# Optimization experiments

Hardware: AMD Instinct MI355X
Metric: run time of the kernel (lower is better)

## Reference

```python
import jax, jax.numpy as jnp
import numpy as np

B, L, D = 4, 1024, 256
N_PER, N_HYP = 48, 16  # n_oscillators=64, n_hyperbolic=16
K = N_PER + N_HYP


def _mlp(x, w1, b1, w2, b2):
    # torch nn.Linear: y = x @ W.T + b; GELU is exact (erf) by default
    h = jax.nn.gelu(x @ w1.T + b1, approximate=False)
    return h @ w2.T + b2


def setup_inputs() -> dict:
    key = jax.random.key(0)
    ks = iter(jax.random.split(key, 32))

    def lin(o, i):
        return jax.random.normal(next(ks), (o, i), jnp.float32) * 0.02

    def bias(o):
        return jnp.zeros((o,), jnp.float32)

    inp = {"x": jax.random.normal(next(ks), (B, L, D), jnp.float32)}
    # key/query periodic phase MLPs: Linear(D,D) -> GELU -> Linear(D,N_PER)
    inp.update(kp_w1=lin(D, D), kp_b1=bias(D), kp_w2=lin(N_PER, D), kp_b2=bias(N_PER))
    inp.update(qp_w1=lin(D, D), qp_b1=bias(D), qp_w2=lin(N_PER, D), qp_b2=bias(N_PER))
    # key/query hyperbolic MLPs: Linear(D,D) -> GELU -> Linear(D, 2*N_HYP)
    inp.update(kh_w1=lin(D, D), kh_b1=bias(D), kh_w2=lin(2 * N_HYP, D), kh_b2=bias(2 * N_HYP))
    inp.update(qh_w1=lin(D, D), qh_b1=bias(D), qh_w2=lin(2 * N_HYP, D), qh_b2=bias(2 * N_HYP))
    # value projection and output (LayerNorm + Linear)
    inp.update(v_w=lin(D, D), v_b=bias(D))
    inp.update(ln_g=jnp.ones((D,), jnp.float32), ln_b=jnp.zeros((D,), jnp.float32))
    inp.update(out_w=lin(D, D), out_b=bias(D))
    return inp


def reference(x, kp_w1, kp_b1, kp_w2, kp_b2, qp_w1, qp_b1, qp_w2, qp_b2,
              kh_w1, kh_b1, kh_w2, kh_b2, qh_w1, qh_b1, qh_w2, qh_b2,
              v_w, v_b, ln_g, ln_b, out_w, out_b):
    Bx, Lx, Dx = x.shape

    # periodic (flat torus) phasors: unit-magnitude
    key_p = jnp.tanh(_mlp(x, kp_w1, kp_b1, kp_w2, kp_b2)) * jnp.pi   # (B,L,N_PER)
    query_p = jnp.tanh(_mlp(x, qp_w1, qp_b1, qp_w2, qp_b2)) * jnp.pi
    key_phasor_p = jnp.exp(1j * key_p.astype(jnp.complex64))
    query_phasor_p = jnp.exp(1j * query_p.astype(jnp.complex64))

    # hyperbolic (Poincare-disk) phasors: amplitude = 1 - |z|
    key_h = jnp.tanh(_mlp(x, kh_w1, kh_b1, kh_w2, kh_b2)).reshape(Bx, Lx, N_HYP, 2) * 0.9
    query_h = jnp.tanh(_mlp(x, qh_w1, qh_b1, qh_w2, qh_b2)).reshape(Bx, Lx, N_HYP, 2) * 0.9
    key_ang = jnp.arctan2(key_h[..., 1], key_h[..., 0])
    query_ang = jnp.arctan2(query_h[..., 1], query_h[..., 0])
    key_amp = 1.0 - jnp.sqrt(jnp.sum(key_h * key_h, axis=-1))
    query_amp = 1.0 - jnp.sqrt(jnp.sum(query_h * query_h, axis=-1))
    key_phasor_h = key_amp * jnp.exp(1j * key_ang.astype(jnp.complex64))
    query_phasor_h = query_amp * jnp.exp(1j * query_ang.astype(jnp.complex64))

    key_phasor = jnp.concatenate([key_phasor_p, key_phasor_h], axis=-1)    # (B,L,K)
    query_phasor = jnp.concatenate([query_phasor_p, query_phasor_h], axis=-1)

    V = (x @ v_w.T + v_b).astype(jnp.complex64)                            # (B,L,D)

    # bind: outer product per timestep, cumsum over L (linear-attention scan)
    bound = key_phasor[..., :, None] * V[..., None, :]                     # (B,L,K,D) complex
    memory = jnp.cumsum(bound, axis=1)
    retrieved = jnp.real(jnp.sum(memory * jnp.conj(query_phasor)[..., None], axis=2))  # (B,L,D)

    positions = jnp.arange(1, Lx + 1, dtype=jnp.float32)
    norm = jnp.sqrt(positions * float(K))[None, :, None]
    r = retrieved / norm

    # to_out: LayerNorm(D) -> Linear(D,D)
    mu = jnp.mean(r, axis=-1, keepdims=True)
    var = jnp.mean(jnp.square(r - mu), axis=-1, keepdims=True)
    r_ln = (r - mu) / jnp.sqrt(var + 1e-5) * ln_g + ln_b
    return x + (r_ln @ out_w.T + out_b)
```

## Files before the change

### kernel.cpp

```cpp
#include <hip/hip_runtime.h>
#include <math.h>


#define Bn 4
#define Ln 1024
#define BLn 4096

typedef __attribute__((ext_vector_type(8))) short bf16x8;
typedef __attribute__((ext_vector_type(4))) float f32x4;

__device__ inline ushort f2bf(float f) {
  union { float f; uint u; } x; x.f = f;
  uint r = x.u + 0x7fffu + ((x.u >> 16) & 1u);
  return (ushort)(r >> 16);
}
__device__ inline uint pk2(float a, float b) {
  return (uint)f2bf(a) | ((uint)f2bf(b) << 16);
}

struct G1Prob { const float* X; const float* W; const float* bias; void* Y; int act; };
struct G1Args { G1Prob p[5]; };

__global__ __launch_bounds__(256) void gemm1(G1Args args) {
  const G1Prob p = args.p[blockIdx.z];
  __shared__ ushort As[64 * 40];
  __shared__ ushort Bs[64 * 40];
  const int tid = threadIdx.x;
  const int m0 = blockIdx.x * 64, n0 = blockIdx.y * 64;
  const int lane = tid & 63, wave = tid >> 6;
  const int wr = wave >> 1, wc = wave & 1;
  const int fr = lane & 15, quad = lane >> 4;
  f32x4 acc[2][2];
#pragma unroll
  for (int i = 0; i < 2; i++)
#pragma unroll
    for (int j = 0; j < 2; j++) acc[i][j] = (f32x4){0.f, 0.f, 0.f, 0.f};

  const int srow = tid >> 2, sch = (tid & 3) * 8;
  for (int k0 = 0; k0 < 256; k0 += 32) {
    float4 a0 = *(const float4*)(p.X + (size_t)(m0 + srow) * 256 + k0 + sch);
    float4 a1 = *(const float4*)(p.X + (size_t)(m0 + srow) * 256 + k0 + sch + 4);
    float4 b0 = *(const float4*)(p.W + (size_t)(n0 + srow) * 256 + k0 + sch);
    float4 b1 = *(const float4*)(p.W + (size_t)(n0 + srow) * 256 + k0 + sch + 4);
    uint4 pa = { pk2(a0.x, a0.y), pk2(a0.z, a0.w), pk2(a1.x, a1.y), pk2(a1.z, a1.w) };
    uint4 pb = { pk2(b0.x, b0.y), pk2(b0.z, b0.w), pk2(b1.x, b1.y), pk2(b1.z, b1.w) };
    *(uint4*)&As[srow * 40 + sch] = pa;
    *(uint4*)&Bs[srow * 40 + sch] = pb;
    __syncthreads();
    bf16x8 fa0 = *(const bf16x8*)&As[(wr * 32 + fr) * 40 + quad * 8];
    bf16x8 fa1 = *(const bf16x8*)&As[(wr * 32 + 16 + fr) * 40 + quad * 8];
    bf16x8 fb0 = *(const bf16x8*)&Bs[(wc * 32 + fr) * 40 + quad * 8];
    bf16x8 fb1 = *(const bf16x8*)&Bs[(wc * 32 + 16 + fr) * 40 + quad * 8];
    acc[0][0] = __builtin_amdgcn_mfma_f32_16x16x32_bf16(fa0, fb0, acc[0][0], 0, 0, 0);
    acc[0][1] = __builtin_amdgcn_mfma_f32_16x16x32_bf16(fa0, fb1, acc[0][1], 0, 0, 0);
    acc[1][0] = __builtin_amdgcn_mfma_f32_16x16x32_bf16(fa1, fb0, acc[1][0], 0, 0, 0);
    acc[1][1] = __builtin_amdgcn_mfma_f32_16x16x32_bf16(fa1, fb1, acc[1][1], 0, 0, 0);
    __syncthreads();
  }
#pragma unroll
  for (int i = 0; i < 2; i++)
#pragma unroll
    for (int j = 0; j < 2; j++) {
      int col = n0 + wc * 32 + j * 16 + fr;
      float bv = p.bias[col];
      if (p.act == 4) {
        int rowg0 = m0 + wr * 32 + i * 16 + quad * 4;
        ushort4 st;
        st.x = f2bf(acc[i][j][0] + bv);
        st.y = f2bf(acc[i][j][1] + bv);
        st.z = f2bf(acc[i][j][2] + bv);
        st.w = f2bf(acc[i][j][3] + bv);
        *(ushort4*)((ushort*)p.Y + (size_t)col * 4096 + rowg0) = st;
      } else {
#pragma unroll
        for (int r = 0; r < 4; r++) {
          int rowg = m0 + wr * 32 + i * 16 + quad * 4 + r;
          float o = acc[i][j][r] + bv;
          o = 0.5f * o * (1.0f + erff(o * 0.70710678118654752f));
          ((ushort*)p.Y)[(size_t)rowg * 256 + col] = f2bf(o);
        }
      }
    }
}

struct G2Prob { const ushort* X; const float* W; const float* bias; float* Y;
                int Nreal; float scale; };
struct G2Args { G2Prob p[4]; };

__global__ __launch_bounds__(256) void gemm2f(G2Args args) {
  const G2Prob p = args.p[blockIdx.z];
  __shared__ ushort As[64 * 40];
  __shared__ ushort Bs[64 * 40];
  const int tid = threadIdx.x;
  const int m0 = blockIdx.x * 64;
  const int lane = tid & 63, wave = tid >> 6;
  const int wr = wave >> 1, wc = wave & 1;
  const int fr = lane & 15, quad = lane >> 4;
  f32x4 acc[2][2];
#pragma unroll
  for (int i = 0; i < 2; i++)
#pragma unroll
    for (int j = 0; j < 2; j++) acc[i][j] = (f32x4){0.f, 0.f, 0.f, 0.f};

  const int srow = tid >> 2, sch = (tid & 3) * 8;
  for (int k0 = 0; k0 < 256; k0 += 32) {
    uint4 pa = *(const uint4*)(p.X + (size_t)(m0 + srow) * 256 + k0 + sch);
    float4 b0 = {0.f,0.f,0.f,0.f}, b1 = {0.f,0.f,0.f,0.f};
    if (srow < p.Nreal) {
      b0 = *(const float4*)(p.W + (size_t)srow * 256 + k0 + sch);
      b1 = *(const float4*)(p.W + (size_t)srow * 256 + k0 + sch + 4);
    }
    uint4 pb = { pk2(b0.x, b0.y), pk2(b0.z, b0.w), pk2(b1.x, b1.y), pk2(b1.z, b1.w) };
    *(uint4*)&As[srow * 40 + sch] = pa;
    *(uint4*)&Bs[srow * 40 + sch] = pb;
    __syncthreads();
    bf16x8 fa0 = *(const bf16x8*)&As[(wr * 32 + fr) * 40 + quad * 8];
    bf16x8 fa1 = *(const bf16x8*)&As[(wr * 32 + 16 + fr) * 40 + quad * 8];
    bf16x8 fb0 = *(const bf16x8*)&Bs[(wc * 32 + fr) * 40 + quad * 8];
    bf16x8 fb1 = *(const bf16x8*)&Bs[(wc * 32 + 16 + fr) * 40 + quad * 8];
    acc[0][0] = __builtin_amdgcn_mfma_f32_16x16x32_bf16(fa0, fb0, acc[0][0], 0, 0, 0);
    acc[0][1] = __builtin_amdgcn_mfma_f32_16x16x32_bf16(fa0, fb1, acc[0][1], 0, 0, 0);
    acc[1][0] = __builtin_amdgcn_mfma_f32_16x16x32_bf16(fa1, fb0, acc[1][0], 0, 0, 0);
    acc[1][1] = __builtin_amdgcn_mfma_f32_16x16x32_bf16(fa1, fb1, acc[1][1], 0, 0, 0);
    __syncthreads();
  }
#pragma unroll
  for (int i = 0; i < 2; i++)
#pragma unroll
    for (int j = 0; j < 2; j++) {
      int col = wc * 32 + j * 16 + fr;
      float bv = (col < p.Nreal) ? p.bias[col] : 0.f;
#pragma unroll
      for (int r = 0; r < 4; r++) {
        int row = m0 + wr * 32 + i * 16 + quad * 4 + r;
        p.Y[(size_t)row * 64 + col] = tanhf(acc[i][j][r] + bv) * p.scale;
      }
    }
}

__global__ __launch_bounds__(256) void phasor_t(const float* kp, const float* qp,
                                                const float* kh, const float* qh,
                                                uint* PhiQ, uint* PhiK, uint* PhiKT) {
  __shared__ ushort LK[64][130];
  const int t = threadIdx.x;
  const int row0 = blockIdx.x * 64;
  const int b = row0 >> 10;
  const int lb0 = row0 & 1023;
#pragma unroll
  for (int it = 0; it < 16; it++) {
    int idx = t + it * 256;
    int k = idx & 63, rl = idx >> 6;
    int row = row0 + rl;
    float kre, kim, qre, qim;
    if (k < 48) {
      float ka = kp[row * 64 + k], qa = qp[row * 64 + k];
      __sincosf(ka, &kim, &kre);
      __sincosf(qa, &qim, &qre);
    } else {
      int j2 = (k - 48) * 2;
      float av = kh[row * 64 + j2], bv = kh[row * 64 + j2 + 1];
      float rr = sqrtf(av * av + bv * bv);
      if (rr > 0.f) { float inv = (1.0f - rr) / rr; kre = av * inv; kim = bv * inv; }
      else          { kre = 1.0f; kim = 0.0f; }
      av = qh[row * 64 + j2]; bv = qh[row * 64 + j2 + 1];
      rr = sqrtf(av * av + bv * bv);
      if (rr > 0.f) { float inv = (1.0f - rr) / rr; qre = av * inv; qim = bv * inv; }
      else          { qre = 1.0f; qim = 0.0f; }
    }
    uint pk = pk2(kre, kim);
    uint pq = pk2(qre, qim);
    PhiK[(size_t)row * 64 + k] = pk;
    PhiQ[(size_t)row * 64 + k] = pq;
    *(uint*)&LK[rl][2 * k] = pk;
  }
  __syncthreads();
#pragma unroll
  for (int it = 0; it < 16; it++) {
    int idx = t + it * 256;
    int k2 = idx >> 5, lp = idx & 31;
    uint v = (uint)LK[lp * 2][k2] | ((uint)LK[lp * 2 + 1][k2] << 16);
    PhiKT[(size_t)b * 65536 + k2 * 512 + (lb0 >> 1) + lp] = v;
  }
}

__global__ __launch_bounds__(256) void kv_chunk(const ushort* VT, const ushort* PhiKT,
                                                float* P) {
  const int bc = blockIdx.x;
  const int b = bc >> 4, c = bc & 15;
  const int d0 = blockIdx.y * 128;
  const int tid = threadIdx.x, lane = tid & 63, wave = tid >> 6;
  const int wr = wave >> 1, wc = wave & 1;
  const int fr = lane & 15, quad = lane >> 4;
  const int colb = b * 1024 + c * 64;
  f32x4 acc[4][4];
#pragma unroll
  for (int i = 0; i < 4; i++)
#pragma unroll
    for (int j = 0; j < 4; j++) acc[i][j] = (f32x4){0.f, 0.f, 0.f, 0.f};
#pragma unroll
  for (int kk = 0; kk < 2; kk++) {
    bf16x8 a[4], bb[4];
#pragma unroll
    for (int i = 0; i < 4; i++)
      a[i] = *(const bf16x8*)(VT + (size_t)(d0 + wr * 64 + i * 16 + fr) * 4096 + colb + kk * 32 + quad * 8);
#pragma unroll
    for (int j = 0; j < 4; j++)
      bb[j] = *(const bf16x8*)(PhiKT + (size_t)b * 131072 + (size_t)(wc * 64 + j * 16 + fr) * 1024 + c * 64 + kk * 32 + quad * 8);
#pragma unroll
    for (int i = 0; i < 4; i++)
#pragma unroll
      for (int j = 0; j < 4; j++)
        acc[i][j] = __builtin_amdgcn_mfma_f32_16x16x32_bf16(a[i], bb[j], acc[i][j], 0, 0, 0);
  }
#pragma unroll
  for (int i = 0; i < 4; i++)
#pragma unroll
    for (int j = 0; j < 4; j++)
#pragma unroll
      for (int r = 0; r < 4; r++) {
        int d = d0 + wr * 64 + i * 16 + quad * 4 + r;
        int k2 = wc * 64 + j * 16 + fr;
        P[((size_t)bc * 256 + d) * 128 + k2] = acc[i][j][r];
      }
}

__global__ void prefix_scan(const float* P, ushort* SpreB) {
  int gid = blockIdx.x * 256 + threadIdx.x;
  int b = gid >> 15, dk = gid & 32767;
  size_t idx = (size_t)b * 16 * 32768 + dk;
  float run = 0.f;
#pragma unroll 4
  for (int c = 0; c < 16; c++) {
    SpreB[idx] = f2bf(run);
    run += P[idx];
    idx += 32768;
  }
}

__global__ __launch_bounds__(256) void retrieve(const ushort* PhiQ, const ushort* PhiK,
                                                const ushort* VT, const ushort* SpreB,
                                                float* R) {
  __shared__ ushort Sl[64 * 72];
  const int bc = blockIdx.x;
  const int b = bc >> 4, c = bc & 15;
  const int d0 = blockIdx.y * 128;
  const int tid = threadIdx.x, lane = tid & 63, wy = tid >> 6;
  const int fr = lane & 15, quad = lane >> 4;
  const int g0 = b * 1024 + c * 64;
  bf16x8 a[4][4];
#pragma unroll
  for (int i = 0; i < 4; i++)
#pragma unroll
    for (int kk = 0; kk < 4; kk++)
      a[i][kk] = *(const bf16x8*)(PhiQ + (size_t)(g0 + i * 16 + fr) * 128 + kk * 32 + quad * 8);

  f32x4 acc[4][2];
#pragma unroll
  for (int i = 0; i < 4; i++)
#pragma unroll
    for (int j = 0; j < 2; j++) acc[i][j] = (f32x4){0.f, 0.f, 0.f, 0.f};

#pragma unroll
  for (int kk = 0; kk < 4; kk++) {
    bf16x8 bb[2];
#pragma unroll
    for (int j = 0; j < 2; j++)
      bb[j] = *(const bf16x8*)(SpreB + ((size_t)bc * 256 + d0 + wy * 32 + j * 16 + fr) * 128 + kk * 32 + quad * 8);
#pragma unroll
    for (int i = 0; i < 4; i++)
#pragma unroll
      for (int j = 0; j < 2; j++)
        acc[i][j] = __builtin_amdgcn_mfma_f32_16x16x32_bf16(a[i][kk], bb[j], acc[i][j], 0, 0, 0);
  }

  f32x4 sacc[4];
#pragma unroll
  for (int i = 0; i < 4; i++) sacc[i] = (f32x4){0.f, 0.f, 0.f, 0.f};
#pragma unroll
  for (int kk = 0; kk < 4; kk++) {
    bf16x8 bs = *(const bf16x8*)(PhiK + (size_t)(g0 + wy * 16 + fr) * 128 + kk * 32 + quad * 8);
#pragma unroll
    for (int i = 0; i < 4; i++)
      sacc[i] = __builtin_amdgcn_mfma_f32_16x16x32_bf16(a[i][kk], bs, sacc[i], 0, 0, 0);
  }
#pragma unroll
  for (int i = 0; i < 4; i++)
#pragma unroll
    for (int r = 0; r < 4; r++) {
      int row = i * 16 + quad * 4 + r;
      int col = wy * 16 + fr;
      Sl[row * 72 + col] = (col <= row) ? f2bf(sacc[i][r]) : (ushort)0;
    }
  __syncthreads();

#pragma unroll
  for (int kk = 0; kk < 2; kk++) {
    bf16x8 as[4], bv[2];
#pragma unroll
    for (int i = 0; i < 4; i++)
      as[i] = *(const bf16x8*)&Sl[(i * 16 + fr) * 72 + kk * 32 + quad * 8];
#pragma unroll
    for (int j = 0; j < 2; j++)
      bv[j] = *(const bf16x8*)(VT + (size_t)(d0 + wy * 32 + j * 16 + fr) * 4096 + g0 + kk * 32 + quad * 8);
#pragma unroll
    for (int i = 0; i < 4; i++)
#pragma unroll
      for (int j = 0; j < 2; j++)
        acc[i][j] = __builtin_amdgcn_mfma_f32_16x16x32_bf16(as[i], bv[j], acc[i][j], 0, 0, 0);
  }

#pragma unroll
  for (int i = 0; i < 4; i++)
#pragma unroll
    for (int j = 0; j < 2; j++)
#pragma unroll
      for (int r = 0; r < 4; r++) {
        int row = i * 16 + quad * 4 + r;
        int d = d0 + wy * 32 + j * 16 + fr;
        float scale = rsqrtf((float)((c * 64 + row + 1) * 64));
        R[(size_t)(g0 + row) * 256 + d] = acc[i][j][r] * scale;
      }
}

__global__ __launch_bounds__(256) void out_ln_gemm(const float* r, const float* g,
                                                   const float* bta, const float* W,
                                                   const float* ob, const float* x,
                                                   float* Y) {
  __shared__ ushort A_lds[64 * 272];
  __shared__ ushort Bs[64 * 40];
  __shared__ float gs[256], bs2[256];
  const int tid = threadIdx.x;
  const int m0 = blockIdx.x * 64, n0 = blockIdx.y * 64;
  gs[tid] = g[tid];
  bs2[tid] = bta[tid];

  const int row_l = tid >> 2, seg = (tid & 3) * 64;
  const float* rr = r + (size_t)(m0 + row_l) * 256 + seg;
  float s = 0.f, sq = 0.f;
#pragma unroll
  for (int i = 0; i < 64; i += 4) {
    float4 v = *(const float4*)(rr + i);
    s += v.x + v.y + v.z + v.w;
    sq += v.x * v.x + v.y * v.y + v.z * v.z + v.w * v.w;
  }
  s += __shfl_xor(s, 1); sq += __shfl_xor(sq, 1);
  s += __shfl_xor(s, 2); sq += __shfl_xor(sq, 2);
  float mean = s * (1.0f / 256.0f);
  float var = fmaxf(sq * (1.0f / 256.0f) - mean * mean, 0.f);
  float rstd = rsqrtf(var + 1e-5f);
  __syncthreads();
#pragma unroll
  for (int i = 0; i < 64; i += 4) {
    float4 v = *(const float4*)(rr + i);
    int k = seg + i;
    ushort4 st;
    st.x = f2bf((v.x - mean) * rstd * gs[k + 0] + bs2[k + 0]);
    st.y = f2bf((v.y - mean) * rstd * gs[k + 1] + bs2[k + 1]);
    st.z = f2bf((v.z - mean) * rstd * gs[k + 2] + bs2[k + 2]);
    st.w = f2bf((v.w - mean) * rstd * gs[k + 3] + bs2[k + 3]);
    *(ushort4*)&A_lds[row_l * 272 + k] = st;
  }
  __syncthreads();

  const int lane = tid & 63, wave = tid >> 6;
  const int wr = wave >> 1, wc = wave & 1;
  const int fr = lane & 15, quad = lane >> 4;
  const int srow = tid >> 2, sch = (tid & 3) * 8;
  f32x4 acc[2][2];
#pragma unroll
  for (int i = 0; i < 2; i++)
#pragma unroll
    for (int j = 0; j < 2; j++) acc[i][j] = (f32x4){0.f, 0.f, 0.f, 0.f};
  for (int k0 = 0; k0 < 256; k0 += 32) {
    float4 b0 = *(const float4*)(W + (size_t)(n0 + srow) * 256 + k0 + sch);
    float4 b1 = *(const float4*)(W + (size_t)(n0 + srow) * 256 + k0 + sch + 4);
    uint4 pb = { pk2(b0.x, b0.y), pk2(b0.z, b0.w), pk2(b1.x, b1.y), pk2(b1.z, b1.w) };
    *(uint4*)&Bs[srow * 40 + sch] = pb;
    __syncthreads();
    bf16x8 fa0 = *(const bf16x8*)&A_lds[(wr * 32 + fr) * 272 + k0 + quad * 8];
    bf16x8 fa1 = *(const bf16x8*)&A_lds[(wr * 32 + 16 + fr) * 272 + k0 + quad * 8];
    bf16x8 fb0 = *(const bf16x8*)&Bs[(wc * 32 + fr) * 40 + quad * 8];
    bf16x8 fb1 = *(const bf16x8*)&Bs[(wc * 32 + 16 + fr) * 40 + quad * 8];
    acc[0][0] = __builtin_amdgcn_mfma_f32_16x16x32_bf16(fa0, fb0, acc[0][0], 0, 0, 0);
    acc[0][1] = __builtin_amdgcn_mfma_f32_16x16x32_bf16(fa0, fb1, acc[0][1], 0, 0, 0);
    acc[1][0] = __builtin_amdgcn_mfma_f32_16x16x32_bf16(fa1, fb0, acc[1][0], 0, 0, 0);
    acc[1][1] = __builtin_amdgcn_mfma_f32_16x16x32_bf16(fa1, fb1, acc[1][1], 0, 0, 0);
    __syncthreads();
  }
#pragma unroll
  for (int i = 0; i < 2; i++)
#pragma unroll
    for (int j = 0; j < 2; j++) {
      int col = n0 + wc * 32 + j * 16 + fr;
      float bv = ob[col];
#pragma unroll
      for (int r = 0; r < 4; r++) {
        int rowg = m0 + wr * 32 + i * 16 + quad * 4 + r;
        Y[(size_t)rowg * 256 + col] = acc[i][j][r] + bv + x[(size_t)rowg * 256 + col];
      }
    }
}

extern "C" void kernel_launch(void* const* d_in, const int* in_sizes, int n_in,
                              void* d_out, int out_size, void* d_ws, size_t ws_size,
                              hipStream_t stream) {
  const float* x     = (const float*)d_in[0];
  const float* kp_w1 = (const float*)d_in[1];
  const float* kp_b1 = (const float*)d_in[2];
  const float* kp_w2 = (const float*)d_in[3];
  const float* kp_b2 = (const float*)d_in[4];
  const float* qp_w1 = (const float*)d_in[5];
  const float* qp_b1 = (const float*)d_in[6];
  const float* qp_w2 = (const float*)d_in[7];
  const float* qp_b2 = (const float*)d_in[8];
  const float* kh_w1 = (const float*)d_in[9];
  const float* kh_b1 = (const float*)d_in[10];
  const float* kh_w2 = (const float*)d_in[11];
  const float* kh_b2 = (const float*)d_in[12];
  const float* qh_w1 = (const float*)d_in[13];
  const float* qh_b1 = (const float*)d_in[14];
  const float* qh_w2 = (const float*)d_in[15];
  const float* qh_b2 = (const float*)d_in[16];
  const float* v_w   = (const float*)d_in[17];
  const float* v_b   = (const float*)d_in[18];
  const float* ln_g  = (const float*)d_in[19];
  const float* ln_b  = (const float*)d_in[20];
  const float* out_w = (const float*)d_in[21];
  const float* out_b = (const float*)d_in[22];

  char* ws = (char*)d_ws;
  const size_t MiB = 1024 * 1024;
  ushort* h0   = (ushort*)(ws + 0);
  ushort* h1   = (ushort*)(ws + 2 * MiB);
  ushort* h2   = (ushort*)(ws + 4 * MiB);
  ushort* h3   = (ushort*)(ws + 6 * MiB);
  ushort* VT   = (ushort*)(ws + 8 * MiB);
  uint*   PhiQ = (uint*)(ws + 10 * MiB);
  uint*   PhiK = (uint*)(ws + 11 * MiB);
  uint*   PhiKT= (uint*)(ws + 12 * MiB);
  float*  kp   = (float*)(ws + 13 * MiB);
  float*  qp   = (float*)(ws + 14 * MiB);
  float*  kh   = (float*)(ws + 15 * MiB);
  float*  qh   = (float*)(ws + 16 * MiB);
  float*  P    = (float*)(ws + 17 * MiB);
  ushort* SpreB= (ushort*)(ws + 25 * MiB);
  float*  r    = (float*)(ws + 29 * MiB);

  G1Args g1;
  g1.p[0] = { x, kp_w1, kp_b1, h0, 1 };
  g1.p[1] = { x, qp_w1, qp_b1, h1, 1 };
  g1.p[2] = { x, kh_w1, kh_b1, h2, 1 };
  g1.p[3] = { x, qh_w1, qh_b1, h3, 1 };
  g1.p[4] = { x, v_w,   v_b,   VT, 4 };
  gemm1<<<dim3(64, 4, 5), 256, 0, stream>>>(g1);

  const float PI_F = 3.14159265358979323846f;
  G2Args g2;
  g2.p[0] = { h0, kp_w2, kp_b2, kp, 48, PI_F };
  g2.p[1] = { h1, qp_w2, qp_b2, qp, 48, PI_F };
  g2.p[2] = { h2, kh_w2, kh_b2, kh, 32, 0.9f };
  g2.p[3] = { h3, qh_w2, qh_b2, qh, 32, 0.9f };
  gemm2f<<<dim3(64, 1, 4), 256, 0, stream>>>(g2);

  phasor_t<<<dim3(64), 256, 0, stream>>>(kp, qp, kh, qh, PhiQ, PhiK, PhiKT);

  kv_chunk<<<dim3(64, 2), 256, 0, stream>>>(VT, (const ushort*)PhiKT, P);

  prefix_scan<<<dim3(512), 256, 0, stream>>>(P, SpreB);

  retrieve<<<dim3(64, 2), 256, 0, stream>>>((const ushort*)PhiQ, (const ushort*)PhiK,
                                            VT, SpreB, r);

  out_ln_gemm<<<dim3(64, 4), 256, 0, stream>>>(r, ln_g, ln_b, out_w, out_b, x,
                                               (float*)d_out);
}
```

Before: 174.1 us.

## Fuse chunk KV outer products and prefix scan into one kernel

Replaces the chunked KV-state MFMA kernel plus the separate prefix-scan kernel with one kernel. Each wave walks the 16 chunks serially, carrying a running fp32 accumulator in registers and writing the exclusive prefix state as bf16. This removes the fp32 P intermediate (8 MiB round trip) and one launch. In exchange it serializes the chunk loop inside each wave, with smaller 16x16 tiles per wave and less MFMA parallelism per block.

```diff
diff --git a/kernel.cpp b/kernel.cpp
--- a/kernel.cpp
+++ b/kernel.cpp
@@ -183,57 +183,32 @@
   }
 }
 
-__global__ __launch_bounds__(256) void kv_chunk(const ushort* VT, const ushort* PhiKT,
-                                                float* P) {
-  const int bc = blockIdx.x;
-  const int b = bc >> 4, c = bc & 15;
-  const int d0 = blockIdx.y * 128;
+__global__ __launch_bounds__(256) void kv_prefix(const ushort* VT, const ushort* PhiKT,
+                                                 ushort* SpreB) {
+  const int b = blockIdx.x >> 4, ds = blockIdx.x & 15;
+  const int d0 = ds * 16;
   const int tid = threadIdx.x, lane = tid & 63, wave = tid >> 6;
-  const int wr = wave >> 1, wc = wave & 1;
   const int fr = lane & 15, quad = lane >> 4;
-  const int colb = b * 1024 + c * 64;
-  f32x4 acc[4][4];
-#pragma unroll
-  for (int i = 0; i < 4; i++)
-#pragma unroll
-    for (int j = 0; j < 4; j++) acc[i][j] = (f32x4){0.f, 0.f, 0.f, 0.f};
-#pragma unroll
-  for (int kk = 0; kk < 2; kk++) {
-    bf16x8 a[4], bb[4];
-#pragma unroll
-    for (int i = 0; i < 4; i++)
-      a[i] = *(const bf16x8*)(VT + (size_t)(d0 + wr * 64 + i * 16 + fr) * 4096 + colb + kk * 32 + quad * 8);
-#pragma unroll
-    for (int j = 0; j < 4; j++)
-      bb[j] = *(const bf16x8*)(PhiKT + (size_t)b * 131072 + (size_t)(wc * 64 + j * 16 + fr) * 1024 + c * 64 + kk * 32 + quad * 8);
-#pragma unroll
-    for (int i = 0; i < 4; i++)
-#pragma unroll
-      for (int j = 0; j < 4; j++)
-        acc[i][j] = __builtin_amdgcn_mfma_f32_16x16x32_bf16(a[i], bb[j], acc[i][j], 0, 0, 0);
-  }
-#pragma unroll
-  for (int i = 0; i < 4; i++)
-#pragma unroll
-    for (int j = 0; j < 4; j++)
-#pragma unroll
-      for (int r = 0; r < 4; r++) {
-        int d = d0 + wr * 64 + i * 16 + quad * 4 + r;
-        int k2 = wc * 64 + j * 16 + fr;
-        P[((size_t)bc * 256 + d) * 128 + k2] = acc[i][j][r];
-      }
-}
-
-__global__ void prefix_scan(const float* P, ushort* SpreB) {
-  int gid = blockIdx.x * 256 + threadIdx.x;
-  int b = gid >> 15, dk = gid & 32767;
-  size_t idx = (size_t)b * 16 * 32768 + dk;
-  float run = 0.f;
+  const int k2b = blockIdx.y * 64 + wave * 16;
+  const ushort* pA = PhiKT + (size_t)b * 131072 + (size_t)(k2b + fr) * 1024;
+  const ushort* pB = VT + (size_t)(d0 + fr) * 4096 + b * 1024;
+  ushort* outp = SpreB + ((size_t)(b * 16) * 256 + d0 + fr) * 128 + k2b + quad * 4;
+  f32x4 carry = (f32x4){0.f, 0.f, 0.f, 0.f};
 #pragma unroll 4
   for (int c = 0; c < 16; c++) {
-    SpreB[idx] = f2bf(run);
-    run += P[idx];
-    idx += 32768;
+    bf16x8 a0 = *(const bf16x8*)(pA + c * 64 + quad * 8);
+    bf16x8 b0 = *(const bf16x8*)(pB + c * 64 + quad * 8);
+    bf16x8 a1 = *(const bf16x8*)(pA + c * 64 + 32 + quad * 8);
+    bf16x8 b1 = *(const bf16x8*)(pB + c * 64 + 32 + quad * 8);
+    ushort4 st;
+    st.x = f2bf(carry[0]); st.y = f2bf(carry[1]);
+    st.z = f2bf(carry[2]); st.w = f2bf(carry[3]);
+    *(ushort4*)outp = st;
+    outp += 32768;
+    f32x4 acc = (f32x4){0.f, 0.f, 0.f, 0.f};
+    acc = __builtin_amdgcn_mfma_f32_16x16x32_bf16(a0, b0, acc, 0, 0, 0);
+    acc = __builtin_amdgcn_mfma_f32_16x16x32_bf16(a1, b1, acc, 0, 0, 0);
+    carry += acc;
   }
 }
 
@@ -442,7 +417,6 @@
   float*  qp   = (float*)(ws + 14 * MiB);
   float*  kh   = (float*)(ws + 15 * MiB);
   float*  qh   = (float*)(ws + 16 * MiB);
-  float*  P    = (float*)(ws + 17 * MiB);
   ushort* SpreB= (ushort*)(ws + 25 * MiB);
   float*  r    = (float*)(ws + 29 * MiB);
 
@@ -464,9 +438,7 @@
 
   phasor_t<<<dim3(64), 256, 0, stream>>>(kp, qp, kh, qh, PhiQ, PhiK, PhiKT);
 
-  kv_chunk<<<dim3(64, 2), 256, 0, stream>>>(VT, (const ushort*)PhiKT, P);
-
-  prefix_scan<<<dim3(512), 256, 0, stream>>>(P, SpreB);
+  kv_prefix<<<dim3(64, 2), 256, 0, stream>>>(VT, (const ushort*)PhiKT, SpreB);
 
   retrieve<<<dim3(64, 2), 256, 0, stream>>>((const ushort*)PhiQ, (const ushort*)PhiK,
                                             VT, SpreB, r);
```

New measurement: 176.3 us. Within noise of the previous version (+1.2%).
